# Performance work log

Hardware: AMD Instinct MI355X
Metric: run time of the kernel (lower is better)

The kernel has to match this reference:

```python
import jax, jax.numpy as jnp
import numpy as np

EPS = 1e-5  # torch BatchNorm1d default eps


def _bn(x, gamma, beta):
    # training-mode BatchNorm1d over the point dimension
    m = jnp.mean(x, axis=0)
    v = jnp.var(x, axis=0)
    return (x - m) * jax.lax.rsqrt(v + EPS) * gamma + beta


def setup_inputs() -> dict:
    key = jax.random.key(0)
    ks = jax.random.split(key, 8)
    N, D = 1000000, 9
    G, V = 32, 32768  # 32^3 voxel grid; with 1M points all voxels occupied w.h.p.
    feats = jax.random.normal(ks[0], (N, D), dtype=jnp.float32)
    coords = jax.random.randint(ks[1], (N, 3), 0, G, dtype=jnp.int32)

    def lin(k, fan_in, fan_out):
        kw, kb = jax.random.split(k)
        s = 1.0 / np.sqrt(fan_in)
        W = jax.random.uniform(kw, (fan_in, fan_out), jnp.float32, -s, s)
        b = jax.random.uniform(kb, (fan_out,), jnp.float32, -s, s)
        return W, b

    W1, b1 = lin(ks[2], 9, 64)
    W2, b2 = lin(ks[3], 64, 128)
    W3, b3 = lin(ks[4], 128, 256)
    W4, b4 = lin(ks[5], 256, 256)
    return {
        'feats': feats, 'coords': coords, 'num_voxels': V,
        'g0': jnp.ones((9,), jnp.float32), 'be0': jnp.zeros((9,), jnp.float32),
        'W1': W1, 'b1': b1,
        'g1': jnp.ones((64,), jnp.float32), 'be1': jnp.zeros((64,), jnp.float32),
        'W2': W2, 'b2': b2,
        'g2': jnp.ones((128,), jnp.float32), 'be2': jnp.zeros((128,), jnp.float32),
        'W3': W3, 'b3': b3,
        'g3': jnp.ones((256,), jnp.float32), 'be3': jnp.zeros((256,), jnp.float32),
        'W4': W4, 'b4': b4,
    }


def _mlp(x, g0, be0, W1, b1, g1, be1, W2, b2, g2, be2, W3, b3, g3, be3, W4, b4):
    x = _bn(x, g0, be0)
    x = jax.nn.relu(_bn(x @ W1 + b1, g1, be1))
    x = jax.nn.relu(_bn(x @ W2 + b2, g2, be2))
    x = jax.nn.relu(_bn(x @ W3 + b3, g3, be3))
    return x @ W4 + b4


def reference(feats, coords, num_voxels, g0, be0, W1, b1, g1, be1, W2, b2,
              g2, be2, W3, b3, g3, be3, W4, b4):
    # NOTE: the torch module shuffles points first; unique(dim=0) is sorted and
    # scatter_max is permutation-invariant, so the shuffle does not affect output.
    unq_coords, unq_inv = jnp.unique(
        coords, axis=0, return_inverse=True, size=num_voxels, fill_value=0)
    unq_inv = unq_inv.reshape(-1)
    unq_coords = unq_coords.astype(jnp.int64)
    h = _mlp(feats, g0, be0, W1, b1, g1, be1, W2, b2, g2, be2, W3, b3, g3, be3, W4, b4)
    pooled = jax.ops.segment_max(h, unq_inv, num_segments=num_voxels)  # [V, 256]
    return pooled, unq_coords
```

## Files before the change

### kernel.cpp

```cpp
#include <hip/hip_runtime.h>
#include <math.h>

#define TPB 256
#define NVOX 32768
#define BN_EPS 1e-5f

typedef short s16x8 __attribute__((ext_vector_type(8)));
typedef short s16x4 __attribute__((ext_vector_type(4)));
typedef float f32x4 __attribute__((ext_vector_type(4)));

#define P0_OFF     0u
#define P1_OFF     256u
#define P2_OFF     (P1_OFF + 64u*128u*4u)
#define P3_OFF     (P2_OFF + 64u*256u*4u)
#define PAR_END    (P3_OFF + 64u*512u*4u)
#define A0_OFF     229632u
#define C0_OFF     229888u
#define A1_OFF     230144u
#define C1_OFF     230400u
#define A2_OFF     230656u
#define C2_OFF     231680u
#define A3_OFF     232704u
#define C3_OFF     233728u
#define HIST_OFF   234752u
#define BASE_OFF   (HIST_OFF + 131072u)
#define CURS_OFF   (BASE_OFF + 131328u)
#define WT1_OFF    (CURS_OFF + 131072u)
#define WT2_OFF    (WT1_OFF + 4096u)
#define WT3_OFF    (WT2_OFF + 16384u)
#define WT4_OFF    (WT3_OFF + 65536u)
#define X_OFF      4845568u

__device__ __forceinline__ unsigned short f2bf(float f) {
    unsigned u = __float_as_uint(f);
    u += 0x7FFFu + ((u >> 16) & 1u);
    return (unsigned short)(u >> 16);
}
__device__ __forceinline__ unsigned short f2bft(float f) {
    return (unsigned short)(__float_as_uint(f) >> 16);
}
__device__ __forceinline__ float bf2f(unsigned short h) {
    return __uint_as_float(((unsigned)h) << 16);
}

template<int ROWB>
__device__ __forceinline__ int swz(int row, int b) {
    constexpr int M = (ROWB >= 128) ? 7 : ((ROWB >= 64) ? 3 : 1);
    return row * ROWB + (b ^ ((row & M) << 4));
}

__device__ __forceinline__ s16x4 bn_relu_pack(f32x4 acc, f32x4 av, f32x4 cv) {
    s16x4 pk;
#pragma unroll
    for (int r = 0; r < 4; ++r) pk[r] = (short)f2bft(fmaxf(fmaf(acc[r], av[r], cv[r]), 0.f));
    return pk;
}

template<int NOUT>
__device__ __forceinline__ void stats_red(f32x4 ps, f32x4 pq, int ch, float* prow) {
#pragma unroll
    for (int m = 1; m <= 8; m <<= 1) {
#pragma unroll
        for (int r = 0; r < 4; ++r) { ps[r] += __shfl_xor(ps[r], m); pq[r] += __shfl_xor(pq[r], m); }
    }
    if ((threadIdx.x & 15) == 0) {
#pragma unroll
        for (int r = 0; r < 4; ++r) {
            atomicAdd(&prow[ch + r], ps[r]);
            atomicAdd(&prow[NOUT + ch + r], pq[r]);
        }
    }
}

__global__ void k_prepw(const float* __restrict__ W1, const float* __restrict__ W2,
                        const float* __restrict__ W3, const float* __restrict__ W4,
                        unsigned short* __restrict__ wt1, unsigned short* __restrict__ wt2,
                        unsigned short* __restrict__ wt3, unsigned short* __restrict__ wt4) {
    for (int i = blockIdx.x * blockDim.x + threadIdx.x; i < 108544;
         i += gridDim.x * blockDim.x) {
        if (i < 2048) {
            int n = i >> 5, k = i & 31;
            wt1[i] = (k < 9) ? f2bf(W1[k * 64 + n]) : (unsigned short)0;
        } else if (i < 10240) {
            int j = i - 2048; int n = j >> 6, k = j & 63;
            wt2[j] = f2bf(W2[k * 128 + n]);
        } else if (i < 43008) {
            int j = i - 10240; int n = j >> 7, k = j & 127;
            wt3[j] = f2bf(W3[k * 256 + n]);
        } else {
            int j = i - 43008; int n = j >> 8, k = j & 255;
            wt4[j] = f2bf(W4[k * 256 + n]);
        }
    }
}

__global__ void k_hist_stats(const int* __restrict__ coords, const float* __restrict__ feats,
                             int N, unsigned* __restrict__ hist, float* __restrict__ banks) {
    float S[9] = {0}, G[45] = {0};
    for (int i = blockIdx.x * blockDim.x + threadIdx.x; i < N;
         i += gridDim.x * blockDim.x) {
        int v = (coords[3 * i] << 10) | (coords[3 * i + 1] << 5) | coords[3 * i + 2];
        atomicAdd(&hist[v], 1u);
        const float* r = feats + (size_t)i * 9;
        float x[9];
#pragma unroll
        for (int c = 0; c < 9; ++c) { x[c] = r[c]; S[c] += x[c]; }
        int idx = 0;
#pragma unroll
        for (int c = 0; c < 9; ++c)
#pragma unroll
            for (int c2 = 0; c2 <= c; ++c2) { G[idx] = fmaf(x[c], x[c2], G[idx]); ++idx; }
    }
#pragma unroll
    for (int m = 1; m <= 32; m <<= 1) {
#pragma unroll
        for (int c = 0; c < 9; ++c) S[c] += __shfl_xor(S[c], m);
#pragma unroll
        for (int j = 0; j < 45; ++j) G[j] += __shfl_xor(G[j], m);
    }
    if ((threadIdx.x & 63) == 0) {
        float* b = banks + (size_t)(blockIdx.x & 63) * 54;
#pragma unroll
        for (int c = 0; c < 9; ++c) atomicAdd(&b[c], S[c]);
#pragma unroll
        for (int j = 0; j < 45; ++j) atomicAdd(&b[9 + j], G[j]);
    }
}

__global__ void k_fin0(const float* __restrict__ banks, float* __restrict__ SG,
                       const float* __restrict__ g0, const float* __restrict__ be0,
                       float* __restrict__ A0, float* __restrict__ C0, float n) {
    __shared__ float sg[54];
    const int t = threadIdx.x;
    if (t < 54) {
        float s = 0.f;
        for (int b = 0; b < 64; ++b) s += banks[b * 54 + t];
        sg[t] = s; SG[t] = s;
    }
    __syncthreads();
    if (t < 9) {
        float m = sg[t] / n;
        float v = sg[9 + t * (t + 1) / 2 + t] / n - m * m;
        float a = g0[t] * rsqrtf(v + BN_EPS);
        A0[t] = a; C0[t] = be0[t] - m * a;
    }
}

__global__ void k_fin1(const float* __restrict__ SG,
                       const float* __restrict__ A0, const float* __restrict__ C0,
                       const float* __restrict__ W1, const float* __restrict__ b1,
                       const float* __restrict__ g1, const float* __restrict__ be1,
                       float* __restrict__ A1, float* __restrict__ C1, float n) {
    __shared__ float Sz[9], Gz[81];
    const int t = threadIdx.x;
    if (t < 9) Sz[t] = A0[t] * SG[t] + n * C0[t];
    if (t < 81) {
        const int c = t / 9, c2 = t - 9 * (t / 9);
        const int i = c > c2 ? c : c2, j = c > c2 ? c2 : c;
        const float G = SG[9 + i * (i + 1) / 2 + j];
        Gz[t] = A0[c] * A0[c2] * G + A0[c] * SG[c] * C0[c2]
              + C0[c] * A0[c2] * SG[c2] + n * C0[c] * C0[c2];
    }
    __syncthreads();
    if (t < 64) {
        float wn[9];
#pragma unroll
        for (int c = 0; c < 9; ++c) wn[c] = W1[c * 64 + t];
        float su = 0.f, qq = 0.f;
#pragma unroll
        for (int c = 0; c < 9; ++c) {
            su = fmaf(wn[c], Sz[c], su);
#pragma unroll
            for (int c2 = 0; c2 < 9; ++c2) qq = fmaf(wn[c] * wn[c2], Gz[c * 9 + c2], qq);
        }
        const float bb = b1[t];
        const float mean = (su + n * bb) / n;
        const float q = qq + 2.f * bb * su + n * bb * bb;
        const float var = q / n - mean * mean;
        const float a = g1[t] * rsqrtf(var + BN_EPS);
        A1[t] = a;
        C1[t] = fmaf(a, bb, be1[t] - mean * a);
    }
}

__global__ void k_scan(const unsigned* __restrict__ hist, int* __restrict__ base,
                       unsigned* __restrict__ cursor, int N) {
    __shared__ unsigned part[1024];
    const int t = threadIdx.x;
    unsigned sum = 0;
    for (int j = 0; j < 32; ++j) sum += hist[t * 32 + j];
    part[t] = sum;
    __syncthreads();
    for (int d = 1; d < 1024; d <<= 1) {
        unsigned v = (t >= d) ? part[t - d] : 0u;
        __syncthreads();
        part[t] += v;
        __syncthreads();
    }
    unsigned run = part[t] - sum;
    for (int j = 0; j < 32; ++j) {
        unsigned h = hist[t * 32 + j];
        base[t * 32 + j] = (int)run;
        cursor[t * 32 + j] = run;
        run += h;
    }
    if (t == 1023) base[32768] = (int)run;
}

__global__ void k_scatter2(const int* __restrict__ coords, const float* __restrict__ feats,
                           int N, unsigned* __restrict__ cursor,
                           const float* __restrict__ A0, const float* __restrict__ C0,
                           unsigned short* __restrict__ Xg) {
    float a0[9], c0[9];
#pragma unroll
    for (int c = 0; c < 9; ++c) { a0[c] = A0[c]; c0[c] = C0[c]; }
    for (int i = blockIdx.x * blockDim.x + threadIdx.x; i < N;
         i += gridDim.x * blockDim.x) {
        int v = (coords[3 * i] << 10) | (coords[3 * i + 1] << 5) | coords[3 * i + 2];
        unsigned pos = atomicAdd(&cursor[v], 1u);
        const float* r = feats + (size_t)i * 9;
        s16x8 lo, hi;
#pragma unroll
        for (int c = 0; c < 8; ++c) lo[c] = (short)f2bf(fmaf(r[c], a0[c], c0[c]));
        hi = (s16x8){0, 0, 0, 0, 0, 0, 0, 0};
        hi[0] = (short)f2bf(fmaf(r[8], a0[8], c0[8]));
        *(s16x8*)(Xg + (size_t)pos * 16) = lo;
        *(s16x8*)(Xg + (size_t)pos * 16 + 8) = hi;
    }
}

__global__ void k_fin(const float* __restrict__ part, int nparts, int C,
                      const float* __restrict__ g, const float* __restrict__ be,
                      const float* __restrict__ bias,
                      float* __restrict__ A, float* __restrict__ Cc, float n) {
    int c = threadIdx.x;
    if (c >= C) return;
    float s = 0.f, q = 0.f;
    for (int r = 0; r < nparts; ++r) { s += part[r * 2 * C + c]; q += part[r * 2 * C + C + c]; }
    float m = s / n;
    float v = q / n - m * m;
    float a = g[c] * rsqrtf(v + BN_EPS);
    float cc = be[c] - m * a;
    A[c] = a;
    Cc[c] = bias ? fmaf(a, bias[c], cc) : cc;
}

__global__ void k_coords(float* __restrict__ outc) {
    int v = blockIdx.x * blockDim.x + threadIdx.x;
    if (v < NVOX) {
        outc[3 * v + 0] = (float)(v >> 10);
        outc[3 * v + 1] = (float)((v >> 5) & 31);
        outc[3 * v + 2] = (float)(v & 31);
    }
}

__global__ __launch_bounds__(256) void k_pass2(
    const unsigned short* __restrict__ Xg,
    const unsigned short* __restrict__ wt1, const unsigned short* __restrict__ wt2,
    const float* __restrict__ A1, const float* __restrict__ C1,
    const float* __restrict__ b2,
    float* __restrict__ p2, int N, int nt) {
    __shared__ char act1[2][16384];
    const int tid = threadIdx.x;
    const int w = tid >> 6, lane = tid & 63, g = lane >> 4, lq = lane & 15;
    const int chb1 = w * 16, chb2 = w * 32;
    const s16x8 a1 = *(const s16x8*)(wt1 + (chb1 + lq) * 32 + g * 8);
    s16x8 w2f[2][2];
#pragma unroll
    for (int mt = 0; mt < 2; ++mt)
#pragma unroll
        for (int kc = 0; kc < 2; ++kc)
            w2f[mt][kc] = *(const s16x8*)(wt2 + (size_t)(chb2 + mt * 16 + lq) * 64 + kc * 32 + g * 8);
    const int ch1 = chb1 + g * 4;
    const f32x4 av1 = *(const f32x4*)(A1 + ch1);
    const f32x4 cv1 = *(const f32x4*)(C1 + ch1);
    f32x4 bv2[2];
#pragma unroll
    for (int mt = 0; mt < 2; ++mt) bv2[mt] = *(const f32x4*)(b2 + chb2 + mt * 16 + g * 4);
    f32x4 ps[2], pq[2];
#pragma unroll
    for (int mt = 0; mt < 2; ++mt) { ps[mt] = (f32x4){0.f,0.f,0.f,0.f}; pq[mt] = (f32x4){0.f,0.f,0.f,0.f}; }

    int t = blockIdx.x;
    if (t < nt) {
#pragma unroll
        for (int ct = 0; ct < 8; ++ct) {
            const int row = ct * 16 + lq;
            const s16x8 b = *(const s16x8*)(Xg + (size_t)(t * 128 + row) * 16 + g * 8);
            f32x4 a = (f32x4){0.f,0.f,0.f,0.f};
            a = __builtin_amdgcn_mfma_f32_16x16x32_bf16(a1, b, a, 0, 0, 0);
            *(s16x4*)(act1[0] + swz<128>(row, ch1 * 2)) = bn_relu_pack(a, av1, cv1);
        }
        __syncthreads();
        int cur = 0;
        while (true) {
            const int tn = t + gridDim.x;
            const bool more = tn < nt;
            const int t0 = t * 128;
            f32x4 acc2[2][8];
#pragma unroll
            for (int mt = 0; mt < 2; ++mt)
#pragma unroll
                for (int ct = 0; ct < 8; ++ct) acc2[mt][ct] = (f32x4){0.f,0.f,0.f,0.f};
#pragma unroll
            for (int kc = 0; kc < 2; ++kc)
#pragma unroll
                for (int ct = 0; ct < 8; ++ct) {
                    const s16x8 b = *(const s16x8*)(act1[cur] + swz<128>(ct * 16 + lq, kc * 64 + g * 16));
#pragma unroll
                    for (int mt = 0; mt < 2; ++mt)
                        acc2[mt][ct] = __builtin_amdgcn_mfma_f32_16x16x32_bf16(w2f[mt][kc], b, acc2[mt][ct], 0, 0, 0);
                }
#pragma unroll
            for (int mt = 0; mt < 2; ++mt)
#pragma unroll
                for (int ct = 0; ct < 8; ++ct) {
                    const bool valid = (t0 + ct * 16 + lq) < N;
#pragma unroll
                    for (int r = 0; r < 4; ++r) {
                        const float h = valid ? (acc2[mt][ct][r] + bv2[mt][r]) : 0.f;
                        ps[mt][r] += h; pq[mt][r] += h * h;
                    }
                }
            if (more) {
#pragma unroll
                for (int ct = 0; ct < 8; ++ct) {
                    const int row = ct * 16 + lq;
                    const s16x8 b = *(const s16x8*)(Xg + (size_t)(tn * 128 + row) * 16 + g * 8);
                    f32x4 a = (f32x4){0.f,0.f,0.f,0.f};
                    a = __builtin_amdgcn_mfma_f32_16x16x32_bf16(a1, b, a, 0, 0, 0);
                    *(s16x4*)(act1[cur ^ 1] + swz<128>(row, ch1 * 2)) = bn_relu_pack(a, av1, cv1);
                }
            }
            __syncthreads();
            if (!more) break;
            t = tn; cur ^= 1;
        }
    }
    float* prow = p2 + (blockIdx.x & 63) * 256;
#pragma unroll
    for (int mt = 0; mt < 2; ++mt)
        stats_red<128>(ps[mt], pq[mt], chb2 + mt * 16 + g * 4, prow);
}

__global__ __launch_bounds__(512) void k_pass3(
    const unsigned short* __restrict__ Xg,
    const unsigned short* __restrict__ wt1, const unsigned short* __restrict__ wt2,
    const unsigned short* __restrict__ wt3,
    const float* __restrict__ A1, const float* __restrict__ C1,
    const float* __restrict__ A2, const float* __restrict__ C2,
    const float* __restrict__ b3,
    float* __restrict__ p3, int N, int nt) {
    __shared__ char act1[8192];
    __shared__ char act2[16384];
    const int tid = threadIdx.x;
    const int w = tid >> 6, lane = tid & 63, g = lane >> 4, lq = lane & 15;
    const int wm = w >> 1, wn = w & 1;
    const int chb1 = wm * 16, chb2 = w * 16, chb3 = w * 32;
    const s16x8 a1 = *(const s16x8*)(wt1 + (chb1 + lq) * 32 + g * 8);
    s16x8 w2f[2], w3f[2][4];
#pragma unroll
    for (int kc = 0; kc < 2; ++kc)
        w2f[kc] = *(const s16x8*)(wt2 + (size_t)(chb2 + lq) * 64 + kc * 32 + g * 8);
#pragma unroll
    for (int mt = 0; mt < 2; ++mt)
#pragma unroll
        for (int kc = 0; kc < 4; ++kc)
            w3f[mt][kc] = *(const s16x8*)(wt3 + (size_t)(chb3 + mt * 16 + lq) * 128 + kc * 32 + g * 8);
    const int ch1 = chb1 + g * 4, ch2 = chb2 + g * 4;
    const f32x4 av1 = *(const f32x4*)(A1 + ch1);
    const f32x4 cv1 = *(const f32x4*)(C1 + ch1);
    const f32x4 av2 = *(const f32x4*)(A2 + ch2);
    const f32x4 cv2 = *(const f32x4*)(C2 + ch2);
    f32x4 bv3[2];
#pragma unroll
    for (int mt = 0; mt < 2; ++mt) bv3[mt] = *(const f32x4*)(b3 + chb3 + mt * 16 + g * 4);
    f32x4 ps[2], pq[2];
#pragma unroll
    for (int mt = 0; mt < 2; ++mt) { ps[mt] = (f32x4){0.f,0.f,0.f,0.f}; pq[mt] = (f32x4){0.f,0.f,0.f,0.f}; }

    int t = blockIdx.x;
    if (t < nt) {
#pragma unroll
        for (int ct = 0; ct < 2; ++ct) {
            const int row = wn * 32 + ct * 16 + lq;
            const s16x8 b = *(const s16x8*)(Xg + (size_t)(t * 64 + row) * 16 + g * 8);
            f32x4 a = (f32x4){0.f,0.f,0.f,0.f};
            a = __builtin_amdgcn_mfma_f32_16x16x32_bf16(a1, b, a, 0, 0, 0);
            *(s16x4*)(act1 + swz<128>(row, ch1 * 2)) = bn_relu_pack(a, av1, cv1);
        }
        __syncthreads();
        {
            f32x4 acc[4];
#pragma unroll
            for (int ct = 0; ct < 4; ++ct) acc[ct] = (f32x4){0.f,0.f,0.f,0.f};
#pragma unroll
            for (int kc = 0; kc < 2; ++kc)
#pragma unroll
                for (int ct = 0; ct < 4; ++ct) {
                    const s16x8 b = *(const s16x8*)(act1 + swz<128>(ct * 16 + lq, kc * 64 + g * 16));
                    acc[ct] = __builtin_amdgcn_mfma_f32_16x16x32_bf16(w2f[kc], b, acc[ct], 0, 0, 0);
                }
#pragma unroll
            for (int ct = 0; ct < 4; ++ct)
                *(s16x4*)(act2 + swz<256>(ct * 16 + lq, ch2 * 2)) = bn_relu_pack(acc[ct], av2, cv2);
        }
        __syncthreads();
        while (true) {
            const int tn = t + gridDim.x;
            const bool more = tn < nt;
            s16x8 xb[2];
            if (more) {
#pragma unroll
                for (int ct = 0; ct < 2; ++ct) {
                    const int row = wn * 32 + ct * 16 + lq;
                    xb[ct] = *(const s16x8*)(Xg + (size_t)(tn * 64 + row) * 16 + g * 8);
                }
            }
            {
                f32x4 acc[2][4];
#pragma unroll
                for (int mt = 0; mt < 2; ++mt)
#pragma unroll
                    for (int ct = 0; ct < 4; ++ct) acc[mt][ct] = (f32x4){0.f,0.f,0.f,0.f};
#pragma unroll
                for (int kc = 0; kc < 4; ++kc)
#pragma unroll
                    for (int ct = 0; ct < 4; ++ct) {
                        const s16x8 b = *(const s16x8*)(act2 + swz<256>(ct * 16 + lq, kc * 64 + g * 16));
#pragma unroll
                        for (int mt = 0; mt < 2; ++mt)
                            acc[mt][ct] = __builtin_amdgcn_mfma_f32_16x16x32_bf16(w3f[mt][kc], b, acc[mt][ct], 0, 0, 0);
                    }
                const int t0 = t * 64;
#pragma unroll
                for (int mt = 0; mt < 2; ++mt)
#pragma unroll
                    for (int ct = 0; ct < 4; ++ct) {
                        const bool valid = (t0 + ct * 16 + lq) < N;
#pragma unroll
                        for (int r = 0; r < 4; ++r) {
                            const float h = valid ? (acc[mt][ct][r] + bv3[mt][r]) : 0.f;
                            ps[mt][r] += h; pq[mt][r] += h * h;
                        }
                    }
            }
            if (more) {
#pragma unroll
                for (int ct = 0; ct < 2; ++ct) {
                    const int row = wn * 32 + ct * 16 + lq;
                    f32x4 a = (f32x4){0.f,0.f,0.f,0.f};
                    a = __builtin_amdgcn_mfma_f32_16x16x32_bf16(a1, xb[ct], a, 0, 0, 0);
                    *(s16x4*)(act1 + swz<128>(row, ch1 * 2)) = bn_relu_pack(a, av1, cv1);
                }
            }
            __syncthreads();
            if (more) {
                f32x4 acc[4];
#pragma unroll
                for (int ct = 0; ct < 4; ++ct) acc[ct] = (f32x4){0.f,0.f,0.f,0.f};
#pragma unroll
                for (int kc = 0; kc < 2; ++kc)
#pragma unroll
                    for (int ct = 0; ct < 4; ++ct) {
                        const s16x8 b = *(const s16x8*)(act1 + swz<128>(ct * 16 + lq, kc * 64 + g * 16));
                        acc[ct] = __builtin_amdgcn_mfma_f32_16x16x32_bf16(w2f[kc], b, acc[ct], 0, 0, 0);
                    }
#pragma unroll
                for (int ct = 0; ct < 4; ++ct)
                    *(s16x4*)(act2 + swz<256>(ct * 16 + lq, ch2 * 2)) = bn_relu_pack(acc[ct], av2, cv2);
            }
            __syncthreads();
            if (!more) break;
            t = tn;
        }
    }
    float* prow = p3 + (blockIdx.x & 63) * 512;
#pragma unroll
    for (int mt = 0; mt < 2; ++mt)
        stats_red<256>(ps[mt], pq[mt], chb3 + mt * 16 + g * 4, prow);
}

__global__ __launch_bounds__(512) void k_pass4(
    const unsigned short* __restrict__ Xg,
    const unsigned short* __restrict__ wt1, const unsigned short* __restrict__ wt2,
    const unsigned short* __restrict__ wt3, const unsigned short* __restrict__ wt4,
    const float* __restrict__ A1, const float* __restrict__ C1,
    const float* __restrict__ A2, const float* __restrict__ C2,
    const float* __restrict__ A3, const float* __restrict__ C3,
    const float* __restrict__ b4,
    const int* __restrict__ base, float* __restrict__ out) {
    extern __shared__ char smem[];
    char* act1 = smem;
    char* act2 = smem + 8192;
    char* act3 = smem + 24576;
    char* h40  = smem + 57344;
    char* h41  = smem + 90112;

    const int tid = threadIdx.x;
    const int w = tid >> 6, lane = tid & 63, g = lane >> 4, lq = lane & 15;
    const int wm = w >> 1, wn = w & 1;
    const int chb1 = wm * 16, chb2 = w * 16, chb = w * 32;
    const int vb = blockIdx.x * 16;
    const int pstart = base[vb], pend = base[vb + 16];
    const int chgrp = tid & 31, slot = tid >> 5;
    const int vlo = base[vb + slot], vhi = base[vb + slot + 1];

    const s16x8 a1 = *(const s16x8*)(wt1 + (chb1 + lq) * 32 + g * 8);
    s16x8 w2f[2], w3f[2][4], w4f[2][8];
#pragma unroll
    for (int kc = 0; kc < 2; ++kc)
        w2f[kc] = *(const s16x8*)(wt2 + (size_t)(chb2 + lq) * 64 + kc * 32 + g * 8);
#pragma unroll
    for (int mt = 0; mt < 2; ++mt) {
#pragma unroll
        for (int kc = 0; kc < 4; ++kc)
            w3f[mt][kc] = *(const s16x8*)(wt3 + (size_t)(chb + mt * 16 + lq) * 128 + kc * 32 + g * 8);
#pragma unroll
        for (int kc = 0; kc < 8; ++kc)
            w4f[mt][kc] = *(const s16x8*)(wt4 + (size_t)(chb + mt * 16 + lq) * 256 + kc * 32 + g * 8);
    }
    const int ch1 = chb1 + g * 4, ch2 = chb2 + g * 4;
    const f32x4 av1 = *(const f32x4*)(A1 + ch1);
    const f32x4 cv1 = *(const f32x4*)(C1 + ch1);
    const f32x4 av2 = *(const f32x4*)(A2 + ch2);
    const f32x4 cv2 = *(const f32x4*)(C2 + ch2);
    f32x4 av3[2], cv3[2], bv4[2];
#pragma unroll
    for (int mt = 0; mt < 2; ++mt) {
        av3[mt] = *(const f32x4*)(A3 + chb + mt * 16 + g * 4);
        cv3[mt] = *(const f32x4*)(C3 + chb + mt * 16 + g * 4);
        bv4[mt] = *(const f32x4*)(b4 + chb + mt * 16 + g * 4);
    }

    float rmax[8];
#pragma unroll
    for (int j = 0; j < 8; ++j) rmax[j] = -INFINITY;

    if (pstart < pend) {
#pragma unroll
        for (int ct = 0; ct < 2; ++ct) {
            const int row = wn * 32 + ct * 16 + lq;
            const s16x8 b = *(const s16x8*)(Xg + (size_t)(pstart + row) * 16 + g * 8);
            f32x4 a = (f32x4){0.f,0.f,0.f,0.f};
            a = __builtin_amdgcn_mfma_f32_16x16x32_bf16(a1, b, a, 0, 0, 0);
            *(s16x4*)(act1 + swz<128>(row, ch1 * 2)) = bn_relu_pack(a, av1, cv1);
        }
        __syncthreads();
        {
            f32x4 acc[4];
#pragma unroll
            for (int ct = 0; ct < 4; ++ct) acc[ct] = (f32x4){0.f,0.f,0.f,0.f};
#pragma unroll
            for (int kc = 0; kc < 2; ++kc)
#pragma unroll
                for (int ct = 0; ct < 4; ++ct) {
                    const s16x8 b = *(const s16x8*)(act1 + swz<128>(ct * 16 + lq, kc * 64 + g * 16));
                    acc[ct] = __builtin_amdgcn_mfma_f32_16x16x32_bf16(w2f[kc], b, acc[ct], 0, 0, 0);
                }
#pragma unroll
            for (int ct = 0; ct < 4; ++ct)
                *(s16x4*)(act2 + swz<256>(ct * 16 + lq, ch2 * 2)) = bn_relu_pack(acc[ct], av2, cv2);
        }
        __syncthreads();

        int cur = 0;
        int lt = pstart;
        for (int t0 = pstart; t0 < pend; t0 += 64) {
            const int nxt = t0 + 64;
            const bool more = nxt < pend;
            char* hcur = cur ? h41 : h40;
            char* hprev = cur ? h40 : h41;
            s16x8 xb0, xb1;
            if (more) {
                xb0 = *(const s16x8*)(Xg + (size_t)(nxt + wn * 32 + lq) * 16 + g * 8);
                xb1 = *(const s16x8*)(Xg + (size_t)(nxt + wn * 32 + 16 + lq) * 16 + g * 8);
            }
#pragma unroll
            for (int mt = 0; mt < 2; ++mt) {
                f32x4 acc[4];
#pragma unroll
                for (int ct = 0; ct < 4; ++ct) acc[ct] = (f32x4){0.f,0.f,0.f,0.f};
#pragma unroll
                for (int kc = 0; kc < 4; ++kc)
#pragma unroll
                    for (int ct = 0; ct < 4; ++ct) {
                        const s16x8 b = *(const s16x8*)(act2 + swz<256>(ct * 16 + lq, kc * 64 + g * 16));
                        acc[ct] = __builtin_amdgcn_mfma_f32_16x16x32_bf16(w3f[mt][kc], b, acc[ct], 0, 0, 0);
                    }
#pragma unroll
                for (int ct = 0; ct < 4; ++ct)
                    *(s16x4*)(act3 + swz<512>(ct * 16 + lq, (chb + mt * 16 + g * 4) * 2)) =
                        bn_relu_pack(acc[ct], av3[mt], cv3[mt]);
            }
            if (more) {
                f32x4 a = (f32x4){0.f,0.f,0.f,0.f};
                a = __builtin_amdgcn_mfma_f32_16x16x32_bf16(a1, xb0, a, 0, 0, 0);
                *(s16x4*)(act1 + swz<128>(wn * 32 + lq, ch1 * 2)) = bn_relu_pack(a, av1, cv1);
                f32x4 a2r = (f32x4){0.f,0.f,0.f,0.f};
                a2r = __builtin_amdgcn_mfma_f32_16x16x32_bf16(a1, xb1, a2r, 0, 0, 0);
                *(s16x4*)(act1 + swz<128>(wn * 32 + 16 + lq, ch1 * 2)) = bn_relu_pack(a2r, av1, cv1);
            }
            __syncthreads();
            if (more) {
                f32x4 acc[4];
#pragma unroll
                for (int ct = 0; ct < 4; ++ct) acc[ct] = (f32x4){0.f,0.f,0.f,0.f};
#pragma unroll
                for (int kc = 0; kc < 2; ++kc)
#pragma unroll
                    for (int ct = 0; ct < 4; ++ct) {
                        const s16x8 b = *(const s16x8*)(act1 + swz<128>(ct * 16 + lq, kc * 64 + g * 16));
                        acc[ct] = __builtin_amdgcn_mfma_f32_16x16x32_bf16(w2f[kc], b, acc[ct], 0, 0, 0);
                    }
#pragma unroll
                for (int ct = 0; ct < 4; ++ct)
                    *(s16x4*)(act2 + swz<256>(ct * 16 + lq, ch2 * 2)) = bn_relu_pack(acc[ct], av2, cv2);
            }
#pragma unroll
            for (int mt = 0; mt < 2; ++mt) {
                f32x4 acc[4];
#pragma unroll
                for (int ct = 0; ct < 4; ++ct) acc[ct] = (f32x4){0.f,0.f,0.f,0.f};
#pragma unroll
                for (int kc = 0; kc < 8; ++kc)
#pragma unroll
                    for (int ct = 0; ct < 4; ++ct) {
                        const s16x8 b = *(const s16x8*)(act3 + swz<512>(ct * 16 + lq, kc * 64 + g * 16));
                        acc[ct] = __builtin_amdgcn_mfma_f32_16x16x32_bf16(w4f[mt][kc], b, acc[ct], 0, 0, 0);
                    }
#pragma unroll
                for (int ct = 0; ct < 4; ++ct) {
                    s16x4 pk;
#pragma unroll
                    for (int r = 0; r < 4; ++r) pk[r] = (short)f2bf(acc[ct][r] + bv4[mt][r]);
                    *(s16x4*)(hcur + swz<512>(ct * 16 + lq, (chb + mt * 16 + g * 4) * 2)) = pk;
                }
            }
            if (t0 > pstart) {
                const int tm = t0 - 64;
                const int lo = max(vlo, tm), hi = min(vhi, tm + 64);
                for (int p = lo; p < hi; ++p) {
                    const s16x8 hv = *(const s16x8*)(hprev + swz<512>(p - tm, chgrp * 16));
#pragma unroll
                    for (int j = 0; j < 8; ++j)
                        rmax[j] = fmaxf(rmax[j], bf2f((unsigned short)hv[j]));
                }
            }
            __syncthreads();
            lt = t0;
            cur ^= 1;
        }
        {
            char* hlast = (cur ^ 1) ? h41 : h40;
            const int lo = max(vlo, lt), hi = min(vhi, lt + 64);
            for (int p = lo; p < hi; ++p) {
                const s16x8 hv = *(const s16x8*)(hlast + swz<512>(p - lt, chgrp * 16));
#pragma unroll
                for (int j = 0; j < 8; ++j)
                    rmax[j] = fmaxf(rmax[j], bf2f((unsigned short)hv[j]));
            }
        }
    }
    float* orow = out + (size_t)(vb + slot) * 256 + chgrp * 8;
    f32x4 o0, o1;
#pragma unroll
    for (int j = 0; j < 4; ++j) { o0[j] = rmax[j]; o1[j] = rmax[4 + j]; }
    *(f32x4*)orow = o0;
    *(f32x4*)(orow + 4) = o1;
}

extern "C" void kernel_launch(void* const* d_in, const int* in_sizes, int n_in,
                              void* d_out, int out_size, void* d_ws, size_t ws_size,
                              hipStream_t stream) {
    const float* feats = (const float*)d_in[0];
    const int* coords = (const int*)d_in[1];
    const float* g0 = (const float*)d_in[3];
    const float* be0 = (const float*)d_in[4];
    const float* W1 = (const float*)d_in[5];
    const float* b1 = (const float*)d_in[6];
    const float* g1 = (const float*)d_in[7];
    const float* be1 = (const float*)d_in[8];
    const float* W2 = (const float*)d_in[9];
    const float* b2 = (const float*)d_in[10];
    const float* g2 = (const float*)d_in[11];
    const float* be2 = (const float*)d_in[12];
    const float* W3 = (const float*)d_in[13];
    const float* b3 = (const float*)d_in[14];
    const float* g3 = (const float*)d_in[15];
    const float* be3 = (const float*)d_in[16];
    const float* W4 = (const float*)d_in[17];
    const float* b4 = (const float*)d_in[18];
    float* out = (float*)d_out;
    char* ws = (char*)d_ws;

    const int N = in_sizes[0] / 9;
    const float fN = (float)N;
    const int nt128 = (N + 127) / 128;
    const int nt64 = (N + 63) / 64;

    unsigned short* Xg = (unsigned short*)(ws + X_OFF);
    const unsigned short* wt1 = (const unsigned short*)(ws + WT1_OFF);
    const unsigned short* wt2 = (const unsigned short*)(ws + WT2_OFF);
    const unsigned short* wt3 = (const unsigned short*)(ws + WT3_OFF);
    const unsigned short* wt4 = (const unsigned short*)(ws + WT4_OFF);
    float* A0 = (float*)(ws + A0_OFF); float* C0 = (float*)(ws + C0_OFF);
    float* A1 = (float*)(ws + A1_OFF); float* C1 = (float*)(ws + C1_OFF);
    float* A2 = (float*)(ws + A2_OFF); float* C2 = (float*)(ws + C2_OFF);
    float* A3 = (float*)(ws + A3_OFF); float* C3 = (float*)(ws + C3_OFF);

    hipMemsetAsync(ws, 0, PAR_END, stream);
    hipMemsetAsync(ws + HIST_OFF, 0, 131072, stream);
    {
        const size_t rows = (size_t)nt128 * 128;
        hipMemsetAsync(ws + X_OFF + (size_t)N * 32u, 0,
                       (rows - (size_t)N) * 32u + 8192u, stream);
    }

    hipFuncSetAttribute((const void*)k_pass4,
        hipFuncAttributeMaxDynamicSharedMemorySize, 122880);

    k_prepw<<<128, TPB, 0, stream>>>(W1, W2, W3, W4,
        (unsigned short*)(ws + WT1_OFF), (unsigned short*)(ws + WT2_OFF),
        (unsigned short*)(ws + WT3_OFF), (unsigned short*)(ws + WT4_OFF));
    k_hist_stats<<<1024, TPB, 0, stream>>>(coords, feats, N,
        (unsigned*)(ws + HIST_OFF), (float*)(ws + P1_OFF));
    k_fin0<<<1, 64, 0, stream>>>((const float*)(ws + P1_OFF), (float*)(ws + P0_OFF),
                                 g0, be0, A0, C0, fN);
    k_fin1<<<1, 128, 0, stream>>>((const float*)(ws + P0_OFF), A0, C0,
                                  W1, b1, g1, be1, A1, C1, fN);
    k_scan<<<1, 1024, 0, stream>>>((const unsigned*)(ws + HIST_OFF),
                                   (int*)(ws + BASE_OFF), (unsigned*)(ws + CURS_OFF), N);
    k_scatter2<<<1024, TPB, 0, stream>>>(coords, feats, N, (unsigned*)(ws + CURS_OFF),
                                         A0, C0, Xg);
    k_coords<<<(NVOX + TPB - 1) / TPB, TPB, 0, stream>>>(out + (size_t)NVOX * 256);

    k_pass2<<<2048, 256, 0, stream>>>(Xg, wt1, wt2, A1, C1, b2,
                                      (float*)(ws + P2_OFF), N, nt128);
    k_fin<<<1, TPB, 0, stream>>>((const float*)(ws + P2_OFF), 64, 128, g2, be2, b2,
                                 A2, C2, fN);

    k_pass3<<<2048, 512, 0, stream>>>(Xg, wt1, wt2, wt3, A1, C1, A2, C2, b3,
                                      (float*)(ws + P3_OFF), N, nt64);
    k_fin<<<1, TPB, 0, stream>>>((const float*)(ws + P3_OFF), 64, 256, g3, be3, b3,
                                 A3, C3, fN);

    k_pass4<<<NVOX / 16, 512, 122880, stream>>>(Xg, wt1, wt2, wt3, wt4,
        A1, C1, A2, C2, A3, C3, b4, (const int*)(ws + BASE_OFF), out);
}
```

Measured before the change: 961.2 us.

## Shrink pass4 tile to 32 points and stream W3/W4 fragments for occupancy

The final fused MLP+segment-max kernel now processes 32 points per iteration instead of 64. It stops keeping the W3/W4 weight fragments resident in registers and reloads them from global memory each iteration with one-step software prefetching. The output buffer is single instead of double, which cuts LDS from 120KB to 44KB, and launch bounds ask for 4 blocks per CU. The aim is higher occupancy and latency hiding, paid for with repeated weight loads from cache and more loop iterations and barriers.

```diff
diff --git a/kernel.cpp b/kernel.cpp
--- a/kernel.cpp
+++ b/kernel.cpp
@@ -481,7 +481,7 @@
         stats_red<256>(ps[mt], pq[mt], chb3 + mt * 16 + g * 4, prow);
 }
 
-__global__ __launch_bounds__(512) void k_pass4(
+__global__ __launch_bounds__(512, 4) void k_pass4(
     const unsigned short* __restrict__ Xg,
     const unsigned short* __restrict__ wt1, const unsigned short* __restrict__ wt2,
     const unsigned short* __restrict__ wt3, const unsigned short* __restrict__ wt4,
@@ -492,10 +492,9 @@
     const int* __restrict__ base, float* __restrict__ out) {
     extern __shared__ char smem[];
     char* act1 = smem;
-    char* act2 = smem + 8192;
-    char* act3 = smem + 24576;
-    char* h40  = smem + 57344;
-    char* h41  = smem + 90112;
+    char* act2 = smem + 4096;
+    char* act3 = smem + 12288;
+    char* h4   = smem + 28672;
 
     const int tid = threadIdx.x;
     const int w = tid >> 6, lane = tid & 63, g = lane >> 4, lq = lane & 15;
@@ -507,19 +506,13 @@
     const int vlo = base[vb + slot], vhi = base[vb + slot + 1];
 
     const s16x8 a1 = *(const s16x8*)(wt1 + (chb1 + lq) * 32 + g * 8);
-    s16x8 w2f[2], w3f[2][4], w4f[2][8];
+    s16x8 w2f[2];
 #pragma unroll
     for (int kc = 0; kc < 2; ++kc)
         w2f[kc] = *(const s16x8*)(wt2 + (size_t)(chb2 + lq) * 64 + kc * 32 + g * 8);
-#pragma unroll
-    for (int mt = 0; mt < 2; ++mt) {
-#pragma unroll
-        for (int kc = 0; kc < 4; ++kc)
-            w3f[mt][kc] = *(const s16x8*)(wt3 + (size_t)(chb + mt * 16 + lq) * 128 + kc * 32 + g * 8);
-#pragma unroll
-        for (int kc = 0; kc < 8; ++kc)
-            w4f[mt][kc] = *(const s16x8*)(wt4 + (size_t)(chb + mt * 16 + lq) * 256 + kc * 32 + g * 8);
-    }
+    const unsigned short* w3p = wt3 + (size_t)(chb + lq) * 128 + g * 8;
+    const unsigned short* w4p = wt4 + (size_t)(chb + lq) * 256 + g * 8;
+
     const int ch1 = chb1 + g * 4, ch2 = chb2 + g * 4;
     const f32x4 av1 = *(const f32x4*)(A1 + ch1);
     const f32x4 cv1 = *(const f32x4*)(C1 + ch1);
@@ -538,9 +531,8 @@
     for (int j = 0; j < 8; ++j) rmax[j] = -INFINITY;
 
     if (pstart < pend) {
-#pragma unroll
-        for (int ct = 0; ct < 2; ++ct) {
-            const int row = wn * 32 + ct * 16 + lq;
+        {
+            const int row = wn * 16 + lq;
             const s16x8 b = *(const s16x8*)(Xg + (size_t)(pstart + row) * 16 + g * 8);
             f32x4 a = (f32x4){0.f,0.f,0.f,0.f};
             a = __builtin_amdgcn_mfma_f32_16x16x32_bf16(a1, b, a, 0, 0, 0);
@@ -548,114 +540,131 @@
         }
         __syncthreads();
         {
-            f32x4 acc[4];
-#pragma unroll
-            for (int ct = 0; ct < 4; ++ct) acc[ct] = (f32x4){0.f,0.f,0.f,0.f};
+            f32x4 acc[2];
+#pragma unroll
+            for (int ct = 0; ct < 2; ++ct) acc[ct] = (f32x4){0.f,0.f,0.f,0.f};
 #pragma unroll
             for (int kc = 0; kc < 2; ++kc)
 #pragma unroll
-                for (int ct = 0; ct < 4; ++ct) {
+                for (int ct = 0; ct < 2; ++ct) {
                     const s16x8 b = *(const s16x8*)(act1 + swz<128>(ct * 16 + lq, kc * 64 + g * 16));
                     acc[ct] = __builtin_amdgcn_mfma_f32_16x16x32_bf16(w2f[kc], b, acc[ct], 0, 0, 0);
                 }
 #pragma unroll
-            for (int ct = 0; ct < 4; ++ct)
+            for (int ct = 0; ct < 2; ++ct)
                 *(s16x4*)(act2 + swz<256>(ct * 16 + lq, ch2 * 2)) = bn_relu_pack(acc[ct], av2, cv2);
         }
         __syncthreads();
 
-        int cur = 0;
         int lt = pstart;
-        for (int t0 = pstart; t0 < pend; t0 += 64) {
-            const int nxt = t0 + 64;
+        for (int t0 = pstart; t0 < pend; t0 += 32) {
+            const int nxt = t0 + 32;
             const bool more = nxt < pend;
-            char* hcur = cur ? h41 : h40;
-            char* hprev = cur ? h40 : h41;
-            s16x8 xb0, xb1;
+            s16x8 xb;
+            if (more)
+                xb = *(const s16x8*)(Xg + (size_t)(nxt + wn * 16 + lq) * 16 + g * 8);
+            {
+                f32x4 acc[2][2];
+#pragma unroll
+                for (int mt = 0; mt < 2; ++mt)
+#pragma unroll
+                    for (int ct = 0; ct < 2; ++ct) acc[mt][ct] = (f32x4){0.f,0.f,0.f,0.f};
+                s16x8 wa0 = *(const s16x8*)(w3p);
+                s16x8 wa1 = *(const s16x8*)(w3p + 2048);
+#pragma unroll
+                for (int kc = 0; kc < 4; ++kc) {
+                    s16x8 wb0, wb1;
+                    if (kc < 3) {
+                        wb0 = *(const s16x8*)(w3p + (kc + 1) * 32);
+                        wb1 = *(const s16x8*)(w3p + 2048 + (kc + 1) * 32);
+                    }
+#pragma unroll
+                    for (int ct = 0; ct < 2; ++ct) {
+                        const s16x8 b = *(const s16x8*)(act2 + swz<256>(ct * 16 + lq, kc * 64 + g * 16));
+                        acc[0][ct] = __builtin_amdgcn_mfma_f32_16x16x32_bf16(wa0, b, acc[0][ct], 0, 0, 0);
+                        acc[1][ct] = __builtin_amdgcn_mfma_f32_16x16x32_bf16(wa1, b, acc[1][ct], 0, 0, 0);
+                    }
+                    wa0 = wb0; wa1 = wb1;
+                }
+#pragma unroll
+                for (int mt = 0; mt < 2; ++mt)
+#pragma unroll
+                    for (int ct = 0; ct < 2; ++ct)
+                        *(s16x4*)(act3 + swz<512>(ct * 16 + lq, (chb + mt * 16 + g * 4) * 2)) =
+                            bn_relu_pack(acc[mt][ct], av3[mt], cv3[mt]);
+            }
+            if (t0 > pstart) {
+                const int tm = t0 - 32;
+                const int lo = max(vlo, tm), hi = min(vhi, tm + 32);
+                for (int p = lo; p < hi; ++p) {
+                    const s16x8 hv = *(const s16x8*)(h4 + swz<512>(p - tm, chgrp * 16));
+#pragma unroll
+                    for (int j = 0; j < 8; ++j)
+                        rmax[j] = fmaxf(rmax[j], bf2f((unsigned short)hv[j]));
+                }
+            }
             if (more) {
-                xb0 = *(const s16x8*)(Xg + (size_t)(nxt + wn * 32 + lq) * 16 + g * 8);
-                xb1 = *(const s16x8*)(Xg + (size_t)(nxt + wn * 32 + 16 + lq) * 16 + g * 8);
-            }
-#pragma unroll
-            for (int mt = 0; mt < 2; ++mt) {
-                f32x4 acc[4];
-#pragma unroll
-                for (int ct = 0; ct < 4; ++ct) acc[ct] = (f32x4){0.f,0.f,0.f,0.f};
-#pragma unroll
-                for (int kc = 0; kc < 4; ++kc)
-#pragma unroll
-                    for (int ct = 0; ct < 4; ++ct) {
-                        const s16x8 b = *(const s16x8*)(act2 + swz<256>(ct * 16 + lq, kc * 64 + g * 16));
-                        acc[ct] = __builtin_amdgcn_mfma_f32_16x16x32_bf16(w3f[mt][kc], b, acc[ct], 0, 0, 0);
-                    }
-#pragma unroll
-                for (int ct = 0; ct < 4; ++ct)
-                    *(s16x4*)(act3 + swz<512>(ct * 16 + lq, (chb + mt * 16 + g * 4) * 2)) =
-                        bn_relu_pack(acc[ct], av3[mt], cv3[mt]);
-            }
-            if (more) {
+                const int row = wn * 16 + lq;
                 f32x4 a = (f32x4){0.f,0.f,0.f,0.f};
-                a = __builtin_amdgcn_mfma_f32_16x16x32_bf16(a1, xb0, a, 0, 0, 0);
-                *(s16x4*)(act1 + swz<128>(wn * 32 + lq, ch1 * 2)) = bn_relu_pack(a, av1, cv1);
-                f32x4 a2r = (f32x4){0.f,0.f,0.f,0.f};
-                a2r = __builtin_amdgcn_mfma_f32_16x16x32_bf16(a1, xb1, a2r, 0, 0, 0);
-                *(s16x4*)(act1 + swz<128>(wn * 32 + 16 + lq, ch1 * 2)) = bn_relu_pack(a2r, av1, cv1);
+                a = __builtin_amdgcn_mfma_f32_16x16x32_bf16(a1, xb, a, 0, 0, 0);
+                *(s16x4*)(act1 + swz<128>(row, ch1 * 2)) = bn_relu_pack(a, av1, cv1);
             }
             __syncthreads();
             if (more) {
-                f32x4 acc[4];
-#pragma unroll
-                for (int ct = 0; ct < 4; ++ct) acc[ct] = (f32x4){0.f,0.f,0.f,0.f};
+                f32x4 acc[2];
+#pragma unroll
+                for (int ct = 0; ct < 2; ++ct) acc[ct] = (f32x4){0.f,0.f,0.f,0.f};
 #pragma unroll
                 for (int kc = 0; kc < 2; ++kc)
 #pragma unroll
-                    for (int ct = 0; ct < 4; ++ct) {
+                    for (int ct = 0; ct < 2; ++ct) {
                         const s16x8 b = *(const s16x8*)(act1 + swz<128>(ct * 16 + lq, kc * 64 + g * 16));
                         acc[ct] = __builtin_amdgcn_mfma_f32_16x16x32_bf16(w2f[kc], b, acc[ct], 0, 0, 0);
                     }
 #pragma unroll
-                for (int ct = 0; ct < 4; ++ct)
+                for (int ct = 0; ct < 2; ++ct)
                     *(s16x4*)(act2 + swz<256>(ct * 16 + lq, ch2 * 2)) = bn_relu_pack(acc[ct], av2, cv2);
             }
-#pragma unroll
-            for (int mt = 0; mt < 2; ++mt) {
-                f32x4 acc[4];
-#pragma unroll
-                for (int ct = 0; ct < 4; ++ct) acc[ct] = (f32x4){0.f,0.f,0.f,0.f};
-#pragma unroll
-                for (int kc = 0; kc < 8; ++kc)
-#pragma unroll
-                    for (int ct = 0; ct < 4; ++ct) {
+            {
+                f32x4 acc[2][2];
+#pragma unroll
+                for (int mt = 0; mt < 2; ++mt)
+#pragma unroll
+                    for (int ct = 0; ct < 2; ++ct) acc[mt][ct] = (f32x4){0.f,0.f,0.f,0.f};
+                s16x8 wa0 = *(const s16x8*)(w4p);
+                s16x8 wa1 = *(const s16x8*)(w4p + 4096);
+#pragma unroll
+                for (int kc = 0; kc < 8; ++kc) {
+                    s16x8 wb0, wb1;
+                    if (kc < 7) {
+                        wb0 = *(const s16x8*)(w4p + (kc + 1) * 32);
+                        wb1 = *(const s16x8*)(w4p + 4096 + (kc + 1) * 32);
+                    }
+#pragma unroll
+                    for (int ct = 0; ct < 2; ++ct) {
                         const s16x8 b = *(const s16x8*)(act3 + swz<512>(ct * 16 + lq, kc * 64 + g * 16));
-                        acc[ct] = __builtin_amdgcn_mfma_f32_16x16x32_bf16(w4f[mt][kc], b, acc[ct], 0, 0, 0);
-                    }
-#pragma unroll
-                for (int ct = 0; ct < 4; ++ct) {
-                    s16x4 pk;
-#pragma unroll
-                    for (int r = 0; r < 4; ++r) pk[r] = (short)f2bf(acc[ct][r] + bv4[mt][r]);
-                    *(s16x4*)(hcur + swz<512>(ct * 16 + lq, (chb + mt * 16 + g * 4) * 2)) = pk;
-                }
-            }
-            if (t0 > pstart) {
-                const int tm = t0 - 64;
-                const int lo = max(vlo, tm), hi = min(vhi, tm + 64);
-                for (int p = lo; p < hi; ++p) {
-                    const s16x8 hv = *(const s16x8*)(hprev + swz<512>(p - tm, chgrp * 16));
-#pragma unroll
-                    for (int j = 0; j < 8; ++j)
-                        rmax[j] = fmaxf(rmax[j], bf2f((unsigned short)hv[j]));
-                }
+                        acc[0][ct] = __builtin_amdgcn_mfma_f32_16x16x32_bf16(wa0, b, acc[0][ct], 0, 0, 0);
+                        acc[1][ct] = __builtin_amdgcn_mfma_f32_16x16x32_bf16(wa1, b, acc[1][ct], 0, 0, 0);
+                    }
+                    wa0 = wb0; wa1 = wb1;
+                }
+#pragma unroll
+                for (int mt = 0; mt < 2; ++mt)
+#pragma unroll
+                    for (int ct = 0; ct < 2; ++ct) {
+                        s16x4 pk;
+#pragma unroll
+                        for (int r = 0; r < 4; ++r) pk[r] = (short)f2bf(acc[mt][ct][r] + bv4[mt][r]);
+                        *(s16x4*)(h4 + swz<512>(ct * 16 + lq, (chb + mt * 16 + g * 4) * 2)) = pk;
+                    }
             }
             __syncthreads();
             lt = t0;
-            cur ^= 1;
         }
         {
-            char* hlast = (cur ^ 1) ? h41 : h40;
-            const int lo = max(vlo, lt), hi = min(vhi, lt + 64);
+            const int lo = max(vlo, lt), hi = min(vhi, lt + 32);
             for (int p = lo; p < hi; ++p) {
-                const s16x8 hv = *(const s16x8*)(hlast + swz<512>(p - lt, chgrp * 16));
+                const s16x8 hv = *(const s16x8*)(h4 + swz<512>(p - lt, chgrp * 16));
 #pragma unroll
                 for (int j = 0; j < 8; ++j)
                     rmax[j] = fmaxf(rmax[j], bf2f((unsigned short)hv[j]));
@@ -718,7 +727,7 @@
     }
 
     hipFuncSetAttribute((const void*)k_pass4,
-        hipFuncAttributeMaxDynamicSharedMemorySize, 122880);
+        hipFuncAttributeMaxDynamicSharedMemorySize, 45056);
 
     k_prepw<<<128, TPB, 0, stream>>>(W1, W2, W3, W4,
         (unsigned short*)(ws + WT1_OFF), (unsigned short*)(ws + WT2_OFF),
@@ -745,6 +754,6 @@
     k_fin<<<1, TPB, 0, stream>>>((const float*)(ws + P3_OFF), 64, 256, g3, be3, b3,
                                  A3, C3, fN);
 
-    k_pass4<<<NVOX / 16, 512, 122880, stream>>>(Xg, wt1, wt2, wt3, wt4,
+    k_pass4<<<NVOX / 16, 512, 45056, stream>>>(Xg, wt1, wt2, wt3, wt4,
         A1, C1, A2, C2, A3, C3, b4, (const int*)(ws + BASE_OFF), out);
 }
```

Measured after the change: 1.457 ms. 1.52x slower.

## Widen pass4 to 1024-thread blocks over 32 voxels with single h4 buffer

Applied to the files above, without the earlier changes.

k_pass4 now runs 16 waves per block, each owning 16 output channels instead of 32, and covers 32 voxels per block. That halves the per-thread weight registers (w3f/w4f) and the MFMA work per wave. The double-buffered layer-4 output is replaced by one buffer, and the segment-max of the previous tile is moved before the next tile's layer-1/2 compute so it can safely reuse that buffer. Shared memory drops to 90 KB, but larger blocks mean more lanes wait at each barrier and the grid has half as many blocks, so load balance across CUs may suffer.

```diff
diff --git a/kernel.cpp b/kernel.cpp
--- a/kernel.cpp
+++ b/kernel.cpp
@@ -481,7 +481,7 @@
         stats_red<256>(ps[mt], pq[mt], chb3 + mt * 16 + g * 4, prow);
 }
 
-__global__ __launch_bounds__(512) void k_pass4(
+__global__ __launch_bounds__(1024, 4) void k_pass4(
     const unsigned short* __restrict__ Xg,
     const unsigned short* __restrict__ wt1, const unsigned short* __restrict__ wt2,
     const unsigned short* __restrict__ wt3, const unsigned short* __restrict__ wt4,
@@ -494,90 +494,75 @@
     char* act1 = smem;
     char* act2 = smem + 8192;
     char* act3 = smem + 24576;
-    char* h40  = smem + 57344;
-    char* h41  = smem + 90112;
+    char* h4   = smem + 57344;
 
     const int tid = threadIdx.x;
     const int w = tid >> 6, lane = tid & 63, g = lane >> 4, lq = lane & 15;
-    const int wm = w >> 1, wn = w & 1;
-    const int chb1 = wm * 16, chb2 = w * 16, chb = w * 32;
-    const int vb = blockIdx.x * 16;
-    const int pstart = base[vb], pend = base[vb + 16];
+    const int c1 = (w & 3) * 16, p1 = (w >> 2) * 16;
+    const int c2 = (w & 7) * 16, p2 = (w >> 3) * 32;
+    const int c3 = w * 16;
+    const int vb = blockIdx.x * 32;
+    const int pstart = base[vb], pend = base[vb + 32];
     const int chgrp = tid & 31, slot = tid >> 5;
     const int vlo = base[vb + slot], vhi = base[vb + slot + 1];
 
-    const s16x8 a1 = *(const s16x8*)(wt1 + (chb1 + lq) * 32 + g * 8);
-    s16x8 w2f[2], w3f[2][4], w4f[2][8];
+    const s16x8 a1 = *(const s16x8*)(wt1 + (c1 + lq) * 32 + g * 8);
+    s16x8 w2f[2], w3f[4], w4f[8];
 #pragma unroll
     for (int kc = 0; kc < 2; ++kc)
-        w2f[kc] = *(const s16x8*)(wt2 + (size_t)(chb2 + lq) * 64 + kc * 32 + g * 8);
-#pragma unroll
-    for (int mt = 0; mt < 2; ++mt) {
-#pragma unroll
-        for (int kc = 0; kc < 4; ++kc)
-            w3f[mt][kc] = *(const s16x8*)(wt3 + (size_t)(chb + mt * 16 + lq) * 128 + kc * 32 + g * 8);
-#pragma unroll
-        for (int kc = 0; kc < 8; ++kc)
-            w4f[mt][kc] = *(const s16x8*)(wt4 + (size_t)(chb + mt * 16 + lq) * 256 + kc * 32 + g * 8);
-    }
-    const int ch1 = chb1 + g * 4, ch2 = chb2 + g * 4;
-    const f32x4 av1 = *(const f32x4*)(A1 + ch1);
-    const f32x4 cv1 = *(const f32x4*)(C1 + ch1);
-    const f32x4 av2 = *(const f32x4*)(A2 + ch2);
-    const f32x4 cv2 = *(const f32x4*)(C2 + ch2);
-    f32x4 av3[2], cv3[2], bv4[2];
-#pragma unroll
-    for (int mt = 0; mt < 2; ++mt) {
-        av3[mt] = *(const f32x4*)(A3 + chb + mt * 16 + g * 4);
-        cv3[mt] = *(const f32x4*)(C3 + chb + mt * 16 + g * 4);
-        bv4[mt] = *(const f32x4*)(b4 + chb + mt * 16 + g * 4);
-    }
+        w2f[kc] = *(const s16x8*)(wt2 + (size_t)(c2 + lq) * 64 + kc * 32 + g * 8);
+#pragma unroll
+    for (int kc = 0; kc < 4; ++kc)
+        w3f[kc] = *(const s16x8*)(wt3 + (size_t)(c3 + lq) * 128 + kc * 32 + g * 8);
+#pragma unroll
+    for (int kc = 0; kc < 8; ++kc)
+        w4f[kc] = *(const s16x8*)(wt4 + (size_t)(c3 + lq) * 256 + kc * 32 + g * 8);
+
+    const f32x4 av1 = *(const f32x4*)(A1 + c1 + g * 4);
+    const f32x4 cv1 = *(const f32x4*)(C1 + c1 + g * 4);
+    const f32x4 av2 = *(const f32x4*)(A2 + c2 + g * 4);
+    const f32x4 cv2 = *(const f32x4*)(C2 + c2 + g * 4);
+    const f32x4 av3 = *(const f32x4*)(A3 + c3 + g * 4);
+    const f32x4 cv3 = *(const f32x4*)(C3 + c3 + g * 4);
+    const f32x4 bv4 = *(const f32x4*)(b4 + c3 + g * 4);
 
     float rmax[8];
 #pragma unroll
     for (int j = 0; j < 8; ++j) rmax[j] = -INFINITY;
 
     if (pstart < pend) {
-#pragma unroll
-        for (int ct = 0; ct < 2; ++ct) {
-            const int row = wn * 32 + ct * 16 + lq;
-            const s16x8 b = *(const s16x8*)(Xg + (size_t)(pstart + row) * 16 + g * 8);
+        {
+            const s16x8 b = *(const s16x8*)(Xg + (size_t)(pstart + p1 + lq) * 16 + g * 8);
             f32x4 a = (f32x4){0.f,0.f,0.f,0.f};
             a = __builtin_amdgcn_mfma_f32_16x16x32_bf16(a1, b, a, 0, 0, 0);
-            *(s16x4*)(act1 + swz<128>(row, ch1 * 2)) = bn_relu_pack(a, av1, cv1);
+            *(s16x4*)(act1 + swz<128>(p1 + lq, (c1 + g * 4) * 2)) = bn_relu_pack(a, av1, cv1);
         }
         __syncthreads();
         {
-            f32x4 acc[4];
-#pragma unroll
-            for (int ct = 0; ct < 4; ++ct) acc[ct] = (f32x4){0.f,0.f,0.f,0.f};
+            f32x4 acc[2];
+#pragma unroll
+            for (int ct = 0; ct < 2; ++ct) acc[ct] = (f32x4){0.f,0.f,0.f,0.f};
 #pragma unroll
             for (int kc = 0; kc < 2; ++kc)
 #pragma unroll
-                for (int ct = 0; ct < 4; ++ct) {
-                    const s16x8 b = *(const s16x8*)(act1 + swz<128>(ct * 16 + lq, kc * 64 + g * 16));
+                for (int ct = 0; ct < 2; ++ct) {
+                    const s16x8 b = *(const s16x8*)(act1 + swz<128>(p2 + ct * 16 + lq, kc * 64 + g * 16));
                     acc[ct] = __builtin_amdgcn_mfma_f32_16x16x32_bf16(w2f[kc], b, acc[ct], 0, 0, 0);
                 }
 #pragma unroll
-            for (int ct = 0; ct < 4; ++ct)
-                *(s16x4*)(act2 + swz<256>(ct * 16 + lq, ch2 * 2)) = bn_relu_pack(acc[ct], av2, cv2);
+            for (int ct = 0; ct < 2; ++ct)
+                *(s16x4*)(act2 + swz<256>(p2 + ct * 16 + lq, (c2 + g * 4) * 2)) = bn_relu_pack(acc[ct], av2, cv2);
         }
         __syncthreads();
 
-        int cur = 0;
         int lt = pstart;
         for (int t0 = pstart; t0 < pend; t0 += 64) {
             const int nxt = t0 + 64;
             const bool more = nxt < pend;
-            char* hcur = cur ? h41 : h40;
-            char* hprev = cur ? h40 : h41;
-            s16x8 xb0, xb1;
-            if (more) {
-                xb0 = *(const s16x8*)(Xg + (size_t)(nxt + wn * 32 + lq) * 16 + g * 8);
-                xb1 = *(const s16x8*)(Xg + (size_t)(nxt + wn * 32 + 16 + lq) * 16 + g * 8);
-            }
-#pragma unroll
-            for (int mt = 0; mt < 2; ++mt) {
+            s16x8 xb;
+            if (more)
+                xb = *(const s16x8*)(Xg + (size_t)(nxt + p1 + lq) * 16 + g * 8);
+            {
                 f32x4 acc[4];
 #pragma unroll
                 for (int ct = 0; ct < 4; ++ct) acc[ct] = (f32x4){0.f,0.f,0.f,0.f};
@@ -586,76 +571,70 @@
 #pragma unroll
                     for (int ct = 0; ct < 4; ++ct) {
                         const s16x8 b = *(const s16x8*)(act2 + swz<256>(ct * 16 + lq, kc * 64 + g * 16));
-                        acc[ct] = __builtin_amdgcn_mfma_f32_16x16x32_bf16(w3f[mt][kc], b, acc[ct], 0, 0, 0);
+                        acc[ct] = __builtin_amdgcn_mfma_f32_16x16x32_bf16(w3f[kc], b, acc[ct], 0, 0, 0);
                     }
 #pragma unroll
                 for (int ct = 0; ct < 4; ++ct)
-                    *(s16x4*)(act3 + swz<512>(ct * 16 + lq, (chb + mt * 16 + g * 4) * 2)) =
-                        bn_relu_pack(acc[ct], av3[mt], cv3[mt]);
-            }
-            if (more) {
-                f32x4 a = (f32x4){0.f,0.f,0.f,0.f};
-                a = __builtin_amdgcn_mfma_f32_16x16x32_bf16(a1, xb0, a, 0, 0, 0);
-                *(s16x4*)(act1 + swz<128>(wn * 32 + lq, ch1 * 2)) = bn_relu_pack(a, av1, cv1);
-                f32x4 a2r = (f32x4){0.f,0.f,0.f,0.f};
-                a2r = __builtin_amdgcn_mfma_f32_16x16x32_bf16(a1, xb1, a2r, 0, 0, 0);
-                *(s16x4*)(act1 + swz<128>(wn * 32 + 16 + lq, ch1 * 2)) = bn_relu_pack(a2r, av1, cv1);
-            }
-            __syncthreads();
-            if (more) {
-                f32x4 acc[4];
-#pragma unroll
-                for (int ct = 0; ct < 4; ++ct) acc[ct] = (f32x4){0.f,0.f,0.f,0.f};
-#pragma unroll
-                for (int kc = 0; kc < 2; ++kc)
-#pragma unroll
-                    for (int ct = 0; ct < 4; ++ct) {
-                        const s16x8 b = *(const s16x8*)(act1 + swz<128>(ct * 16 + lq, kc * 64 + g * 16));
-                        acc[ct] = __builtin_amdgcn_mfma_f32_16x16x32_bf16(w2f[kc], b, acc[ct], 0, 0, 0);
-                    }
-#pragma unroll
-                for (int ct = 0; ct < 4; ++ct)
-                    *(s16x4*)(act2 + swz<256>(ct * 16 + lq, ch2 * 2)) = bn_relu_pack(acc[ct], av2, cv2);
-            }
-#pragma unroll
-            for (int mt = 0; mt < 2; ++mt) {
-                f32x4 acc[4];
-#pragma unroll
-                for (int ct = 0; ct < 4; ++ct) acc[ct] = (f32x4){0.f,0.f,0.f,0.f};
-#pragma unroll
-                for (int kc = 0; kc < 8; ++kc)
-#pragma unroll
-                    for (int ct = 0; ct < 4; ++ct) {
-                        const s16x8 b = *(const s16x8*)(act3 + swz<512>(ct * 16 + lq, kc * 64 + g * 16));
-                        acc[ct] = __builtin_amdgcn_mfma_f32_16x16x32_bf16(w4f[mt][kc], b, acc[ct], 0, 0, 0);
-                    }
-#pragma unroll
-                for (int ct = 0; ct < 4; ++ct) {
-                    s16x4 pk;
-#pragma unroll
-                    for (int r = 0; r < 4; ++r) pk[r] = (short)f2bf(acc[ct][r] + bv4[mt][r]);
-                    *(s16x4*)(hcur + swz<512>(ct * 16 + lq, (chb + mt * 16 + g * 4) * 2)) = pk;
-                }
+                    *(s16x4*)(act3 + swz<512>(ct * 16 + lq, (c3 + g * 4) * 2)) =
+                        bn_relu_pack(acc[ct], av3, cv3);
             }
             if (t0 > pstart) {
                 const int tm = t0 - 64;
                 const int lo = max(vlo, tm), hi = min(vhi, tm + 64);
                 for (int p = lo; p < hi; ++p) {
-                    const s16x8 hv = *(const s16x8*)(hprev + swz<512>(p - tm, chgrp * 16));
+                    const s16x8 hv = *(const s16x8*)(h4 + swz<512>(p - tm, chgrp * 16));
 #pragma unroll
                     for (int j = 0; j < 8; ++j)
                         rmax[j] = fmaxf(rmax[j], bf2f((unsigned short)hv[j]));
                 }
             }
+            if (more) {
+                f32x4 a = (f32x4){0.f,0.f,0.f,0.f};
+                a = __builtin_amdgcn_mfma_f32_16x16x32_bf16(a1, xb, a, 0, 0, 0);
+                *(s16x4*)(act1 + swz<128>(p1 + lq, (c1 + g * 4) * 2)) = bn_relu_pack(a, av1, cv1);
+            }
+            __syncthreads();
+            if (more) {
+                f32x4 acc[2];
+#pragma unroll
+                for (int ct = 0; ct < 2; ++ct) acc[ct] = (f32x4){0.f,0.f,0.f,0.f};
+#pragma unroll
+                for (int kc = 0; kc < 2; ++kc)
+#pragma unroll
+                    for (int ct = 0; ct < 2; ++ct) {
+                        const s16x8 b = *(const s16x8*)(act1 + swz<128>(p2 + ct * 16 + lq, kc * 64 + g * 16));
+                        acc[ct] = __builtin_amdgcn_mfma_f32_16x16x32_bf16(w2f[kc], b, acc[ct], 0, 0, 0);
+                    }
+#pragma unroll
+                for (int ct = 0; ct < 2; ++ct)
+                    *(s16x4*)(act2 + swz<256>(p2 + ct * 16 + lq, (c2 + g * 4) * 2)) = bn_relu_pack(acc[ct], av2, cv2);
+            }
+            {
+                f32x4 acc[4];
+#pragma unroll
+                for (int ct = 0; ct < 4; ++ct) acc[ct] = (f32x4){0.f,0.f,0.f,0.f};
+#pragma unroll
+                for (int kc = 0; kc < 8; ++kc)
+#pragma unroll
+                    for (int ct = 0; ct < 4; ++ct) {
+                        const s16x8 b = *(const s16x8*)(act3 + swz<512>(ct * 16 + lq, kc * 64 + g * 16));
+                        acc[ct] = __builtin_amdgcn_mfma_f32_16x16x32_bf16(w4f[kc], b, acc[ct], 0, 0, 0);
+                    }
+#pragma unroll
+                for (int ct = 0; ct < 4; ++ct) {
+                    s16x4 pk;
+#pragma unroll
+                    for (int r = 0; r < 4; ++r) pk[r] = (short)f2bf(acc[ct][r] + bv4[r]);
+                    *(s16x4*)(h4 + swz<512>(ct * 16 + lq, (c3 + g * 4) * 2)) = pk;
+                }
+            }
             __syncthreads();
             lt = t0;
-            cur ^= 1;
         }
         {
-            char* hlast = (cur ^ 1) ? h41 : h40;
             const int lo = max(vlo, lt), hi = min(vhi, lt + 64);
             for (int p = lo; p < hi; ++p) {
-                const s16x8 hv = *(const s16x8*)(hlast + swz<512>(p - lt, chgrp * 16));
+                const s16x8 hv = *(const s16x8*)(h4 + swz<512>(p - lt, chgrp * 16));
 #pragma unroll
                 for (int j = 0; j < 8; ++j)
                     rmax[j] = fmaxf(rmax[j], bf2f((unsigned short)hv[j]));
@@ -718,7 +697,7 @@
     }
 
     hipFuncSetAttribute((const void*)k_pass4,
-        hipFuncAttributeMaxDynamicSharedMemorySize, 122880);
+        hipFuncAttributeMaxDynamicSharedMemorySize, 90112);
 
     k_prepw<<<128, TPB, 0, stream>>>(W1, W2, W3, W4,
         (unsigned short*)(ws + WT1_OFF), (unsigned short*)(ws + WT2_OFF),
@@ -745,6 +724,6 @@
     k_fin<<<1, TPB, 0, stream>>>((const float*)(ws + P3_OFF), 64, 256, g3, be3, b3,
                                  A3, C3, fN);
 
-    k_pass4<<<NVOX / 16, 512, 122880, stream>>>(Xg, wt1, wt2, wt3, wt4,
+    k_pass4<<<NVOX / 32, 1024, 90112, stream>>>(Xg, wt1, wt2, wt3, wt4,
         A1, C1, A2, C2, A3, C3, b4, (const int*)(ws + BASE_OFF), out);
 }
```

Result: faster. 938.9 us (-2.3%).
